# Kernel optimization log

Hardware: AMD Instinct MI355X
Metric: run time of the kernel (lower is better)

## Reference

```python
import jax, jax.numpy as jnp
import numpy as np

T, B, I, H, L = 512, 32, 256, 512, 3  # seq_len, batch, input_size, hidden_size, num_layers


def setup_inputs() -> dict:
    key = jax.random.key(0)
    ks = jax.random.split(key, 2 + 2 * L)
    d = {}
    d["x"] = jax.random.normal(ks[0], (T, B, I), dtype=jnp.float32)
    d["h0"] = jax.random.normal(ks[1], (2 * L, B, H), dtype=jnp.float32)
    in_dims = [I, 2 * H, 2 * H]
    for l in range(L):
        k_ih, k_hh = jax.random.split(ks[2 + l], 2)
        d[f"w_ih{l}"] = jax.random.normal(k_ih, (2, in_dims[l], 3 * H), dtype=jnp.float32) * np.float32(1.0 / np.sqrt(in_dims[l]))
        d[f"w_hh{l}"] = jax.random.normal(k_hh, (2, H, 3 * H), dtype=jnp.float32) * np.float32(1.0 / np.sqrt(H))
        d[f"b_ih{l}"] = jnp.zeros((2, 3 * H), dtype=jnp.float32)
        d[f"b_hh{l}"] = jnp.zeros((2, 3 * H), dtype=jnp.float32)
    return d


def _gru_direction(xs, h0d, w_ih, w_hh, b_ih, b_hh, reverse):
    # xs: (T, B, in_dim). Precompute all input-side gates in one big GEMM.
    gi = jnp.einsum('tbi,ig->tbg', xs, w_ih) + b_ih  # (T, B, 3H)

    def step(h, g):
        gh = h @ w_hh + b_hh                         # (B, 3H)
        i_r, i_z, i_n = jnp.split(g, 3, axis=-1)
        h_r, h_z, h_n = jnp.split(gh, 3, axis=-1)
        r = jax.nn.sigmoid(i_r + h_r)
        z = jax.nn.sigmoid(i_z + h_z)
        n = jnp.tanh(i_n + r * h_n)
        h_new = (1.0 - z) * n + z * h
        return h_new, h_new

    _, ys = jax.lax.scan(step, h0d, gi, reverse=reverse)
    return ys  # (T, B, H), aligned with input time order


def reference(x, h0, w_ih0, w_hh0, b_ih0, b_hh0,
              w_ih1, w_hh1, b_ih1, b_hh1,
              w_ih2, w_hh2, b_ih2, b_hh2):
    params = [(w_ih0, w_hh0, b_ih0, b_hh0),
              (w_ih1, w_hh1, b_ih1, b_hh1),
              (w_ih2, w_hh2, b_ih2, b_hh2)]
    layer_in = x
    for l, (w_ih, w_hh, b_ih, b_hh) in enumerate(params):
        fwd = _gru_direction(layer_in, h0[2 * l], w_ih[0], w_hh[0], b_ih[0], b_hh[0], reverse=False)
        bwd = _gru_direction(layer_in, h0[2 * l + 1], w_ih[1], w_hh[1], b_ih[1], b_hh[1], reverse=True)
        layer_in = jnp.concatenate([fwd, bwd], axis=-1)  # (T, B, 2H)
    return layer_in
```

## Files before the change

kernel.cpp:

```cpp
#include <hip/hip_runtime.h>

#define T_LEN 512
#define BATCH 32
#define HSZ 512
#define G3 1536
#define MROWS 16384

typedef unsigned int u32;
typedef unsigned long long u64;
typedef unsigned short u16;
typedef __attribute__((ext_vector_type(8))) short bf16x8;
typedef __attribute__((ext_vector_type(4))) float f32x4;

static __device__ __forceinline__ u16 f2bf(float x) {
  u32 u = __float_as_uint(x);
  u32 r = (u + 0x7FFFu + ((u >> 16) & 1u)) >> 16;
  return (u16)r;
}
static __device__ __forceinline__ u32 pack_bf16(float a, float b) {
  return (u32)f2bf(a) | ((u32)f2bf(b) << 16);
}
static __device__ __forceinline__ float nz(float x) { return (x == x) ? x : 0.f; }

__global__ __launch_bounds__(256) void transpose_bf16(
    const float* __restrict__ src, u16* __restrict__ dst, int K, int N)
{
  int dirz = blockIdx.z;
  src += (size_t)dirz * K * N;
  dst += (size_t)dirz * N * K;
  __shared__ float tile[32][33];
  int n0 = blockIdx.x * 32, k0 = blockIdx.y * 32;
  int tx = threadIdx.x & 31, ty = threadIdx.x >> 5;
#pragma unroll
  for (int i = ty; i < 32; i += 8)
    tile[i][tx] = src[(size_t)(k0 + i) * N + n0 + tx];
  __syncthreads();
#pragma unroll
  for (int i = ty; i < 32; i += 8)
    dst[(size_t)(n0 + i) * K + k0 + tx] = f2bf(tile[tx][i]);
}

__global__ __launch_bounds__(256) void convert_x(
    const float* __restrict__ src, u16* __restrict__ dst, int n4)
{
  int i = blockIdx.x * 256 + threadIdx.x;
  if (i >= n4) return;
  float4 v = ((const float4*)src)[i];
  union { u16 h[4]; uint2 u; } o;
  o.h[0] = f2bf(v.x); o.h[1] = f2bf(v.y); o.h[2] = f2bf(v.z); o.h[3] = f2bf(v.w);
  ((uint2*)dst)[i] = o.u;
}

__global__ __launch_bounds__(256) void gemm_gi(
    const u16* __restrict__ A,
    const u16* __restrict__ Bw,
    const float* __restrict__ bias,
    _Float16* __restrict__ C,
    int M, int K)
{
  const int N = G3;
  int dir = blockIdx.z;
  const u16* Bd = Bw + (size_t)dir * N * K;
  _Float16* Cd = C + (size_t)dir * N * M;
  const float* biasd = bias + dir * N;

  int tm = blockIdx.x * 128;
  int tn = blockIdx.y * 128;

  __shared__ u16 sA[128][40];
  __shared__ u16 sB[128][40];

  int tid = threadIdx.x;
  int lane = tid & 63, wave = tid >> 6;
  int wm = (wave & 1) << 6, wn = (wave >> 1) << 6;

  f32x4 acc[4][4] = {};

  int srow = tid >> 1, shalf = (tid & 1) << 4;
  const u16* pa = A + (size_t)(tm + srow) * K + shalf;
  const u16* pb = Bd + (size_t)(tn + srow) * K + shalf;

  for (int k0 = 0; k0 < K; k0 += 32) {
    uint4 va0 = *(const uint4*)(pa + k0);
    uint4 va1 = *(const uint4*)(pa + k0 + 8);
    uint4 vb0 = *(const uint4*)(pb + k0);
    uint4 vb1 = *(const uint4*)(pb + k0 + 8);
    *(uint4*)&sA[srow][shalf]     = va0;
    *(uint4*)&sA[srow][shalf + 8] = va1;
    *(uint4*)&sB[srow][shalf]     = vb0;
    *(uint4*)&sB[srow][shalf + 8] = vb1;
    __syncthreads();
    int kg = (lane >> 4) << 3;
    int r16 = lane & 15;
    bf16x8 af[4], bfr[4];
#pragma unroll
    for (int f = 0; f < 4; f++) {
      af[f]  = *(const bf16x8*)&sA[wm + f * 16 + r16][kg];
      bfr[f] = *(const bf16x8*)&sB[wn + f * 16 + r16][kg];
    }
#pragma unroll
    for (int fm = 0; fm < 4; fm++)
#pragma unroll
      for (int fn = 0; fn < 4; fn++)
        acc[fm][fn] = __builtin_amdgcn_mfma_f32_16x16x32_bf16(af[fm], bfr[fn], acc[fm][fn], 0, 0, 0);
    __syncthreads();
  }

  int col4 = lane & 15, rbase = (lane >> 4) << 2;
#pragma unroll
  for (int fn = 0; fn < 4; fn++) {
    int col = tn + wn + fn * 16 + col4;
    float bv = biasd[col];
#pragma unroll
    for (int fm = 0; fm < 4; fm++) {
      int row0 = tm + wm + fm * 16 + rbase;
      union { _Float16 h[4]; uint2 u; } o;
#pragma unroll
      for (int r = 0; r < 4; r++)
        o.h[r] = (_Float16)nz(acc[fm][fn][r] + bv);
      *(uint2*)&Cd[(size_t)col * M + row0] = o.u;
    }
  }
}

__global__ __launch_bounds__(64, 1) void gru_rec(
    const _Float16* __restrict__ gi,
    const u16* __restrict__ whhT,
    const float* __restrict__ bhh,
    const float* __restrict__ h0,
    float* __restrict__ outF,
    u16* __restrict__ outB,
    u32* __restrict__ hbuf,
    int* __restrict__ flags,
    int base)
{
  int dir = blockIdx.x >> 5;
  int jc  = blockIdx.x & 31;
  int lane = threadIdx.x;
  int l15 = lane & 15;
  int q   = lane >> 4;
  int j   = jc * 16 + l15;

  __shared__ u16 sWf[3 * 16 * 64 * 8];

#pragma unroll
  for (int it = 0; it < 48; it++) {
    int g = it >> 4, kg = it & 15;
    const u16* src = whhT + ((size_t)dir * G3 + g * 512 + jc * 16 + l15) * HSZ + kg * 32 + q * 8;
    *(uint4*)&sWf[(it * 64 + lane) * 8] = *(const uint4*)src;
  }
  __syncthreads();

  float bhr = bhh[dir * G3 + j];
  float bhz = bhh[dir * G3 + 512 + j];
  float bhn = bhh[dir * G3 + 1024 + j];

  float hm[8];
#pragma unroll
  for (int mt = 0; mt < 2; mt++)
#pragma unroll
    for (int r = 0; r < 4; r++)
      hm[mt * 4 + r] = h0[((size_t)dir * BATCH + mt * 16 + q * 4 + r) * HSZ + j];

  {
    u32* hb = hbuf + (size_t)dir * (BATCH * HSZ / 2);
#pragma unroll
    for (int i = 0; i < 8; i++) {
      int b = (i >> 2) * 16 + q * 4 + (i & 3);
      float partner = __shfl_xor(hm[i], 1);
      if (!(l15 & 1))
        __hip_atomic_store(&hb[(size_t)b * (HSZ / 2) + (j >> 1)], pack_bf16(hm[i], partner),
                           __ATOMIC_RELAXED, __HIP_MEMORY_SCOPE_AGENT);
    }
  }
  __builtin_amdgcn_fence(__ATOMIC_RELEASE, "workgroup");
  __builtin_amdgcn_s_waitcnt(0);
  if (lane == 0)
    __hip_atomic_store(&flags[(dir * 32 + jc) * 16], base + 1,
                       __ATOMIC_RELAXED, __HIP_MEMORY_SCOPE_AGENT);
  __builtin_amdgcn_sched_barrier(0);

  uint2 gir[2][3][2];
  {
    int te0 = dir ? (T_LEN - 1) : 0;
#pragma unroll
    for (int g = 0; g < 3; g++) {
      const _Float16* gb = gi + ((size_t)dir * G3 + g * 512 + j) * MROWS + (size_t)te0 * BATCH;
      gir[0][g][0] = *(const uint2*)(gb + q * 4);
      gir[0][g][1] = *(const uint2*)(gb + 16 + q * 4);
    }
  }

  for (int t2 = 0; t2 < T_LEN; t2 += 2) {
#pragma unroll
    for (int p = 0; p < 2; p++) {
      const int t = t2 + p;
      const int t_eff = dir ? (T_LEN - 1 - t) : t;

      {
        const int target = base + t + 1;
        const int* fl = &flags[(dir * 32 + (lane & 31)) * 16];
        while (true) {
          int f;
          asm volatile("flat_load_dword %0, %1 sc0 sc1\n\t"
                       "s_waitcnt lgkmcnt(0)"
                       : "=&v"(f) : "v"(fl) : "memory");
          __builtin_amdgcn_sched_barrier(0);
          if (__ballot(f >= target) == ~0ull) break;
        }
      }

      const u32* hc = hbuf + ((size_t)(t & 1) * 2 + dir) * (BATCH * HSZ / 2);
      union { u64 q[2]; bf16x8 v; } a0[16], a1[16];
#pragma unroll
      for (int kg = 0; kg < 16; kg++) {
        const u32* p0 = hc + (size_t)l15 * (HSZ / 2) + kg * 16 + q * 4;
        const u32* p1 = hc + (size_t)(16 + l15) * (HSZ / 2) + kg * 16 + q * 4;
        a0[kg].q[0] = __hip_atomic_load((const u64*)p0,       __ATOMIC_RELAXED, __HIP_MEMORY_SCOPE_AGENT);
        a0[kg].q[1] = __hip_atomic_load((const u64*)(p0 + 2), __ATOMIC_RELAXED, __HIP_MEMORY_SCOPE_AGENT);
        a1[kg].q[0] = __hip_atomic_load((const u64*)p1,       __ATOMIC_RELAXED, __HIP_MEMORY_SCOPE_AGENT);
        a1[kg].q[1] = __hip_atomic_load((const u64*)(p1 + 2), __ATOMIC_RELAXED, __HIP_MEMORY_SCOPE_AGENT);
      }

      f32x4 aR0 = {}, aR1 = {}, aZ0 = {}, aZ1 = {}, aN0 = {}, aN1 = {};
#pragma unroll
      for (int kg = 0; kg < 16; kg++) {
        bf16x8 wR = *(const bf16x8*)&sWf[((0 * 16 + kg) * 64 + lane) * 8];
        bf16x8 wZ = *(const bf16x8*)&sWf[((1 * 16 + kg) * 64 + lane) * 8];
        bf16x8 wN = *(const bf16x8*)&sWf[((2 * 16 + kg) * 64 + lane) * 8];
        aR0 = __builtin_amdgcn_mfma_f32_16x16x32_bf16(a0[kg].v, wR, aR0, 0, 0, 0);
        aR1 = __builtin_amdgcn_mfma_f32_16x16x32_bf16(a1[kg].v, wR, aR1, 0, 0, 0);
        aZ0 = __builtin_amdgcn_mfma_f32_16x16x32_bf16(a0[kg].v, wZ, aZ0, 0, 0, 0);
        aZ1 = __builtin_amdgcn_mfma_f32_16x16x32_bf16(a1[kg].v, wZ, aZ1, 0, 0, 0);
        aN0 = __builtin_amdgcn_mfma_f32_16x16x32_bf16(a0[kg].v, wN, aN0, 0, 0, 0);
        aN1 = __builtin_amdgcn_mfma_f32_16x16x32_bf16(a1[kg].v, wN, aN1, 0, 0, 0);
      }

      float hv[8];
#pragma unroll
      for (int mt = 0; mt < 2; mt++)
#pragma unroll
        for (int r = 0; r < 4; r++) {
          int i = mt * 4 + r;
          union { uint2 u; _Float16 h[4]; } cr, cz, cn;
          cr.u = gir[p][0][mt]; cz.u = gir[p][1][mt]; cn.u = gir[p][2][mt];
          float aR = mt ? aR1[r] : aR0[r];
          float aZ = mt ? aZ1[r] : aZ0[r];
          float aN = mt ? aN1[r] : aN0[r];
          float xr = (float)cr.h[r] + aR + bhr;
          float xz = (float)cz.h[r] + aZ + bhz;
          xr = fminf(fmaxf(xr, -40.f), 40.f);
          xz = fminf(fmaxf(xz, -40.f), 40.f);
          float rr = __builtin_amdgcn_rcpf(1.f + __expf(-xr));
          float zz = __builtin_amdgcn_rcpf(1.f + __expf(-xz));
          float xn = (float)cn.h[r] + rr * (aN + bhn);
          xn = fminf(fmaxf(xn, -15.f), 15.f);
          float e2 = __expf(2.f * xn);
          float nn = (e2 - 1.f) * __builtin_amdgcn_rcpf(e2 + 1.f);
          hv[i] = (1.f - zz) * nn + zz * hm[i];
          hm[i] = hv[i];
        }

      u32* hn = hbuf + ((size_t)((t + 1) & 1) * 2 + dir) * (BATCH * HSZ / 2);
#pragma unroll
      for (int i = 0; i < 8; i++) {
        int b = (i >> 2) * 16 + q * 4 + (i & 3);
        float partner = __shfl_xor(hv[i], 1);
        if (!(l15 & 1))
          __hip_atomic_store(&hn[(size_t)b * (HSZ / 2) + (j >> 1)], pack_bf16(hv[i], partner),
                             __ATOMIC_RELAXED, __HIP_MEMORY_SCOPE_AGENT);
      }
      __builtin_amdgcn_fence(__ATOMIC_RELEASE, "workgroup");
      __builtin_amdgcn_s_waitcnt(0);
      if (lane == 0)
        __hip_atomic_store(&flags[(dir * 32 + jc) * 16], base + t + 2,
                           __ATOMIC_RELAXED, __HIP_MEMORY_SCOPE_AGENT);
      __builtin_amdgcn_sched_barrier(0);

      if (t + 1 < T_LEN) {
        int te1 = dir ? (T_LEN - 2 - t) : t + 1;
#pragma unroll
        for (int g = 0; g < 3; g++) {
          const _Float16* gb = gi + ((size_t)dir * G3 + g * 512 + j) * MROWS + (size_t)te1 * BATCH;
          gir[p ^ 1][g][0] = *(const uint2*)(gb + q * 4);
          gir[p ^ 1][g][1] = *(const uint2*)(gb + 16 + q * 4);
        }
      }

#pragma unroll
      for (int i = 0; i < 8; i++) {
        int b = (i >> 2) * 16 + q * 4 + (i & 3);
        size_t oidx = ((size_t)t_eff * BATCH + b) * 1024 + dir * HSZ + j;
        if (outF) outF[oidx] = hv[i];
        if (outB) outB[oidx] = f2bf(hv[i]);
      }
    }
  }
}

extern "C" void kernel_launch(void* const* d_in, const int* in_sizes, int n_in,
                              void* d_out, int out_size, void* d_ws, size_t ws_size,
                              hipStream_t stream)
{
  const float* x  = (const float*)d_in[0];
  const float* h0 = (const float*)d_in[1];
  const float* w_ih[3] = {(const float*)d_in[2], (const float*)d_in[6], (const float*)d_in[10]};
  const float* w_hh[3] = {(const float*)d_in[3], (const float*)d_in[7], (const float*)d_in[11]};
  const float* b_ih[3] = {(const float*)d_in[4], (const float*)d_in[8], (const float*)d_in[12]};
  const float* b_hh[3] = {(const float*)d_in[5], (const float*)d_in[9], (const float*)d_in[13]};

  char* ws = (char*)d_ws;
  size_t off = 0;
  auto alloc = [&](size_t bytes) {
    void* p = ws + off;
    off = (off + bytes + 255) & ~(size_t)255;
    return p;
  };
  int* flags = (int*)alloc(4096);
  u32* hbuf = (u32*)alloc((size_t)2 * 2 * BATCH * (HSZ / 2) * 4);
  u16* xbf  = (u16*)alloc((size_t)16384 * 256 * 2);
  u16* lobf = (u16*)alloc((size_t)16384 * 1024 * 2);
  u16* wihT[3];
  wihT[0] = (u16*)alloc((size_t)2 * G3 * 256 * 2);
  wihT[1] = (u16*)alloc((size_t)2 * G3 * 1024 * 2);
  wihT[2] = (u16*)alloc((size_t)2 * G3 * 1024 * 2);
  u16* whhT[3];
  for (int l = 0; l < 3; l++) whhT[l] = (u16*)alloc((size_t)2 * G3 * 512 * 2);
  _Float16* gi = (_Float16*)alloc((size_t)2 * T_LEN * BATCH * G3 * 2);

  hipMemsetAsync(flags, 0, 4096, stream);

  convert_x<<<4096, 256, 0, stream>>>(x, xbf, 16384 * 256 / 4);
  transpose_bf16<<<dim3(48, 8, 2),  256, 0, stream>>>(w_ih[0], wihT[0], 256,  G3);
  transpose_bf16<<<dim3(48, 32, 2), 256, 0, stream>>>(w_ih[1], wihT[1], 1024, G3);
  transpose_bf16<<<dim3(48, 32, 2), 256, 0, stream>>>(w_ih[2], wihT[2], 1024, G3);
  for (int l = 0; l < 3; l++)
    transpose_bf16<<<dim3(48, 16, 2), 256, 0, stream>>>(w_hh[l], whhT[l], 512, G3);

  const int M = T_LEN * BATCH;
  for (int l = 0; l < 3; l++) {
    int K = (l == 0) ? 256 : 1024;
    const u16* Ain = (l == 0) ? xbf : lobf;
    gemm_gi<<<dim3(M / 128, G3 / 128, 2), 256, 0, stream>>>(Ain, wihT[l], b_ih[l], gi, M, K);
    float* oF = (l == 2) ? (float*)d_out : nullptr;
    u16* oB = (l < 2) ? lobf : nullptr;
    gru_rec<<<64, 64, 0, stream>>>(gi, whhT[l], b_hh[l],
                                   h0 + (size_t)l * 2 * BATCH * HSZ,
                                   oF, oB, hbuf, flags, l * 513);
  }
}
```

Before: 6.697 ms.

## Replace flag-based step sync with parity bits embedded in hidden-state data

Removes the per-step flag array, the release fence, the waitcnt and the flag spin-loop. Each packed bf16 pair now carries a parity bit in its low mantissa bit, and stores are widened to 64-bit units. Readers spin on the hidden-state loads themselves until every word shows the expected parity. This cuts a flag round trip and fence latency from the serial recurrence chain, at the cost of one bit of bf16 precision. It relies on 64-bit atomic stores being seen whole and on the buffer being initialised to 0xFF.

Result: slower. 9.325 ms (+39.2%).

```diff
diff --git a/kernel.cpp b/kernel.cpp
--- a/kernel.cpp
+++ b/kernel.cpp
@@ -131,7 +131,6 @@
     float* __restrict__ outF,
     u16* __restrict__ outB,
     u32* __restrict__ hbuf,
-    int* __restrict__ flags,
     int base)
 {
   int dir = blockIdx.x >> 5;
@@ -163,22 +162,22 @@
       hm[mt * 4 + r] = h0[((size_t)dir * BATCH + mt * 16 + q * 4 + r) * HSZ + j];
 
   {
-    u32* hb = hbuf + (size_t)dir * (BATCH * HSZ / 2);
+    u32 seq0 = (u32)base;
+    u32 slot = seq0 & 1, par = (seq0 >> 1) & 1;
+    u32* hb = hbuf + ((size_t)slot * 2 + dir) * (BATCH * HSZ / 2);
 #pragma unroll
     for (int i = 0; i < 8; i++) {
       int b = (i >> 2) * 16 + q * 4 + (i & 3);
       float partner = __shfl_xor(hm[i], 1);
-      if (!(l15 & 1))
-        __hip_atomic_store(&hb[(size_t)b * (HSZ / 2) + (j >> 1)], pack_bf16(hm[i], partner),
+      u32 pk = (pack_bf16(hm[i], partner) & ~1u) | par;
+      u32 pk2 = (u32)__shfl_xor((int)pk, 2);
+      if ((l15 & 3) == 0) {
+        u64 unit = (u64)pk | ((u64)pk2 << 32);
+        __hip_atomic_store((u64*)&hb[(size_t)b * (HSZ / 2) + (j >> 1)], unit,
                            __ATOMIC_RELAXED, __HIP_MEMORY_SCOPE_AGENT);
-    }
-  }
-  __builtin_amdgcn_fence(__ATOMIC_RELEASE, "workgroup");
-  __builtin_amdgcn_s_waitcnt(0);
-  if (lane == 0)
-    __hip_atomic_store(&flags[(dir * 32 + jc) * 16], base + 1,
-                       __ATOMIC_RELAXED, __HIP_MEMORY_SCOPE_AGENT);
-  __builtin_amdgcn_sched_barrier(0);
+      }
+    }
+  }
 
   uint2 gir[2][3][2];
   {
@@ -197,29 +196,31 @@
       const int t = t2 + p;
       const int t_eff = dir ? (T_LEN - 1 - t) : t;
 
-      {
-        const int target = base + t + 1;
-        const int* fl = &flags[(dir * 32 + (lane & 31)) * 16];
-        while (true) {
-          int f;
-          asm volatile("flat_load_dword %0, %1 sc0 sc1\n\t"
-                       "s_waitcnt lgkmcnt(0)"
-                       : "=&v"(f) : "v"(fl) : "memory");
-          __builtin_amdgcn_sched_barrier(0);
-          if (__ballot(f >= target) == ~0ull) break;
-        }
-      }
-
-      const u32* hc = hbuf + ((size_t)(t & 1) * 2 + dir) * (BATCH * HSZ / 2);
-      union { u64 q[2]; bf16x8 v; } a0[16], a1[16];
-#pragma unroll
-      for (int kg = 0; kg < 16; kg++) {
-        const u32* p0 = hc + (size_t)l15 * (HSZ / 2) + kg * 16 + q * 4;
-        const u32* p1 = hc + (size_t)(16 + l15) * (HSZ / 2) + kg * 16 + q * 4;
-        a0[kg].q[0] = __hip_atomic_load((const u64*)p0,       __ATOMIC_RELAXED, __HIP_MEMORY_SCOPE_AGENT);
-        a0[kg].q[1] = __hip_atomic_load((const u64*)(p0 + 2), __ATOMIC_RELAXED, __HIP_MEMORY_SCOPE_AGENT);
-        a1[kg].q[0] = __hip_atomic_load((const u64*)p1,       __ATOMIC_RELAXED, __HIP_MEMORY_SCOPE_AGENT);
-        a1[kg].q[1] = __hip_atomic_load((const u64*)(p1 + 2), __ATOMIC_RELAXED, __HIP_MEMORY_SCOPE_AGENT);
+      const u32 seq  = (u32)base + (u32)t;
+      const u32 slot = seq & 1;
+      const u32 par  = (seq >> 1) & 1;
+      const u32* hc = hbuf + ((size_t)slot * 2 + dir) * (BATCH * HSZ / 2);
+      union HU { u64 qq[2]; bf16x8 v; } a0[16], a1[16];
+      while (true) {
+#pragma unroll
+        for (int kg = 0; kg < 16; kg++) {
+          const u32* p0 = hc + (size_t)l15 * (HSZ / 2) + kg * 16 + q * 4;
+          const u32* p1 = hc + (size_t)(16 + l15) * (HSZ / 2) + kg * 16 + q * 4;
+          a0[kg].qq[0] = __hip_atomic_load((const u64*)p0,       __ATOMIC_RELAXED, __HIP_MEMORY_SCOPE_AGENT);
+          a0[kg].qq[1] = __hip_atomic_load((const u64*)(p0 + 2), __ATOMIC_RELAXED, __HIP_MEMORY_SCOPE_AGENT);
+          a1[kg].qq[0] = __hip_atomic_load((const u64*)p1,       __ATOMIC_RELAXED, __HIP_MEMORY_SCOPE_AGENT);
+          a1[kg].qq[1] = __hip_atomic_load((const u64*)(p1 + 2), __ATOMIC_RELAXED, __HIP_MEMORY_SCOPE_AGENT);
+        }
+        u32 acc = par ? ~0u : 0u;
+#pragma unroll
+        for (int kg = 0; kg < 16; kg++) {
+          u32 w00 = (u32)a0[kg].qq[0], w01 = (u32)a0[kg].qq[1];
+          u32 w10 = (u32)a1[kg].qq[0], w11 = (u32)a1[kg].qq[1];
+          if (par) acc &= (w00 & w01 & w10 & w11);
+          else     acc |= (w00 | w01 | w10 | w11);
+        }
+        bool ok = ((acc & 1u) == par);
+        if (__ballot(ok) == ~0ull) break;
       }
 
       f32x4 aR0 = {}, aR1 = {}, aZ0 = {}, aZ1 = {}, aN0 = {}, aN1 = {};
@@ -261,21 +262,23 @@
           hm[i] = hv[i];
         }
 
-      u32* hn = hbuf + ((size_t)((t + 1) & 1) * 2 + dir) * (BATCH * HSZ / 2);
-#pragma unroll
-      for (int i = 0; i < 8; i++) {
-        int b = (i >> 2) * 16 + q * 4 + (i & 3);
-        float partner = __shfl_xor(hv[i], 1);
-        if (!(l15 & 1))
-          __hip_atomic_store(&hn[(size_t)b * (HSZ / 2) + (j >> 1)], pack_bf16(hv[i], partner),
-                             __ATOMIC_RELAXED, __HIP_MEMORY_SCOPE_AGENT);
-      }
-      __builtin_amdgcn_fence(__ATOMIC_RELEASE, "workgroup");
-      __builtin_amdgcn_s_waitcnt(0);
-      if (lane == 0)
-        __hip_atomic_store(&flags[(dir * 32 + jc) * 16], base + t + 2,
-                           __ATOMIC_RELAXED, __HIP_MEMORY_SCOPE_AGENT);
-      __builtin_amdgcn_sched_barrier(0);
+      {
+        u32 seq1 = (u32)base + (u32)t + 1;
+        u32 slot1 = seq1 & 1, par1 = (seq1 >> 1) & 1;
+        u32* hn = hbuf + ((size_t)slot1 * 2 + dir) * (BATCH * HSZ / 2);
+#pragma unroll
+        for (int i = 0; i < 8; i++) {
+          int b = (i >> 2) * 16 + q * 4 + (i & 3);
+          float partner = __shfl_xor(hv[i], 1);
+          u32 pk = (pack_bf16(hv[i], partner) & ~1u) | par1;
+          u32 pk2 = (u32)__shfl_xor((int)pk, 2);
+          if ((l15 & 3) == 0) {
+            u64 unit = (u64)pk | ((u64)pk2 << 32);
+            __hip_atomic_store((u64*)&hn[(size_t)b * (HSZ / 2) + (j >> 1)], unit,
+                               __ATOMIC_RELAXED, __HIP_MEMORY_SCOPE_AGENT);
+          }
+        }
+      }
 
       if (t + 1 < T_LEN) {
         int te1 = dir ? (T_LEN - 2 - t) : t + 1;
@@ -316,7 +319,6 @@
     off = (off + bytes + 255) & ~(size_t)255;
     return p;
   };
-  int* flags = (int*)alloc(4096);
   u32* hbuf = (u32*)alloc((size_t)2 * 2 * BATCH * (HSZ / 2) * 4);
   u16* xbf  = (u16*)alloc((size_t)16384 * 256 * 2);
   u16* lobf = (u16*)alloc((size_t)16384 * 1024 * 2);
@@ -328,7 +330,7 @@
   for (int l = 0; l < 3; l++) whhT[l] = (u16*)alloc((size_t)2 * G3 * 512 * 2);
   _Float16* gi = (_Float16*)alloc((size_t)2 * T_LEN * BATCH * G3 * 2);
 
-  hipMemsetAsync(flags, 0, 4096, stream);
+  hipMemsetAsync(hbuf, 0xFF, (size_t)2 * 2 * BATCH * (HSZ / 2) * 4, stream);
 
   convert_x<<<4096, 256, 0, stream>>>(x, xbf, 16384 * 256 / 4);
   transpose_bf16<<<dim3(48, 8, 2),  256, 0, stream>>>(w_ih[0], wihT[0], 256,  G3);
@@ -346,6 +348,6 @@
     u16* oB = (l < 2) ? lobf : nullptr;
     gru_rec<<<64, 64, 0, stream>>>(gi, whhT[l], b_hh[l],
                                    h0 + (size_t)l * 2 * BATCH * HSZ,
-                                   oF, oB, hbuf, flags, l * 513);
-  }
-}
+                                   oF, oB, hbuf, l * 513);
+  }
+}
```
